# Optimization experiments

Measured on AMD Instinct MI355X. Metric: run time of the kernel, lower is better.

## Reference

```python
import jax, jax.numpy as jnp
import numpy as np

B, C, W, H = 4, 256, 64, 64
CQK = C // 8  # 32


def setup_inputs() -> dict:
    key = jax.random.key(0)
    ks = jax.random.split(key, 8)
    scale = 0.02
    x = jax.random.normal(ks[0], (B, C, W, H), dtype=jnp.float32)
    wq = jax.random.normal(ks[1], (CQK, C), dtype=jnp.float32) * scale
    bq = jnp.zeros((CQK,), dtype=jnp.float32)
    wk = jax.random.normal(ks[2], (CQK, C), dtype=jnp.float32) * scale
    bk = jnp.zeros((CQK,), dtype=jnp.float32)
    wv = jax.random.normal(ks[3], (C, C), dtype=jnp.float32) * scale
    bv = jnp.zeros((C,), dtype=jnp.float32)
    gamma = jnp.zeros((1,), dtype=jnp.float32)
    return {"x": x, "wq": wq, "bq": bq, "wk": wk, "bk": bk,
            "wv": wv, "bv": bv, "gamma": gamma}


def reference(x, wq, bq, wk, bk, wv, bv, gamma):
    b, c, w, h = x.shape
    n = w * h
    xf = x.reshape(b, c, n)                         # b, C, N
    # 1x1 convs == channel matmuls
    q = jnp.einsum('oc,bcn->bno', wq, xf) + bq      # b, N, Cqk
    k = jnp.einsum('oc,bcn->bon', wk, xf) + bk[:, None]  # b, Cqk, N
    v = jnp.einsum('oc,bcn->bon', wv, xf) + bv[:, None]  # b, C, N
    energy = jnp.einsum('bic,bcj->bij', q, k)       # b, N, N
    attention = jax.nn.softmax(energy, axis=-1)     # b, N, N
    # out[b,c,i] = sum_j v[b,c,j] * attention[b,i,j]
    out = jnp.einsum('bcj,bij->bci', v, attention)  # b, C, N
    out = out.reshape(b, c, w, h)
    out = gamma[0] * out + x
    return out, attention
```

## Files before the change

### kernel.cpp

```cpp
#include <hip/hip_runtime.h>

#define NB 4
#define NC 256
#define NN 4096
#define NQK 32

typedef short short8 __attribute__((ext_vector_type(8)));
typedef float f32x4 __attribute__((ext_vector_type(4)));

#define MFMA16(a, b, c) __builtin_amdgcn_mfma_f32_16x16x32_bf16((a), (b), (c), 0, 0, 0)

#if __has_builtin(__builtin_amdgcn_exp2f)
#define EXP2(x) __builtin_amdgcn_exp2f(x)
#else
#define EXP2(x) __expf((x) * 0.6931471805599453f)
#endif

#define L2E 1.4426950408889634f

__device__ __forceinline__ unsigned short f2bf(float f) {
  unsigned int u = __builtin_bit_cast(unsigned int, f);
  u += 0x7fffu + ((u >> 16) & 1u);
  return (unsigned short)(u >> 16);
}
__device__ __forceinline__ float bf2f(unsigned short u) {
  unsigned int v = ((unsigned int)u) << 16;
  return __builtin_bit_cast(float, v);
}

__global__ void k_prep(const float* __restrict__ wq, const float* __restrict__ wk,
                       const float* __restrict__ wv,
                       unsigned short* __restrict__ wqb, unsigned short* __restrict__ wkb,
                       unsigned short* __restrict__ wvb) {
  int i = blockIdx.x * 256 + threadIdx.x;
  if (i < NQK * NC) { wqb[i] = f2bf(wq[i]); wkb[i] = f2bf(wk[i]); }
  wvb[i] = f2bf(wv[i]);
}

__global__ __launch_bounds__(256) void k_proj(
    const float* __restrict__ x,
    const unsigned short* __restrict__ wqb, const unsigned short* __restrict__ wkb,
    const unsigned short* __restrict__ wvb,
    const float* __restrict__ bq, const float* __restrict__ bk,
    const float* __restrict__ bv,
    unsigned short* __restrict__ qb, unsigned short* __restrict__ kTb,
    unsigned short* __restrict__ vb) {
  __shared__ unsigned short ldsx[32][264];
  __shared__ unsigned short ldsvt[256][40];
  int b = blockIdx.y, n0 = blockIdx.x * 32;
  int t = threadIdx.x, w = t >> 6, l = t & 63, lm = l & 15, lk = l >> 4;
  const float* xb = x + (size_t)b * NC * NN + n0;
#pragma unroll
  for (int p = 0; p < 8; ++p) {
    int c = p * 32 + (t >> 3);
    int n4 = (t & 7) * 4;
    f32x4 v4 = *(const f32x4*)(xb + (size_t)c * NN + n4);
#pragma unroll
    for (int u = 0; u < 4; ++u) ldsx[n4 + u][c] = f2bf(v4[u]);
  }
  __syncthreads();
  int s = w & 1, h = w >> 1;
  f32x4 qa[2] = {}, ka[2] = {}, va[10] = {};
  if (h == 0) {
#pragma unroll
    for (int kk = 0; kk < 8; ++kk) {
      short8 a = *(const short8*)(&ldsx[s * 16 + lm][kk * 32 + lk * 8]);
      const unsigned short* wqp = wqb + lm * NC + kk * 32 + lk * 8;
      const unsigned short* wkp = wkb + lm * NC + kk * 32 + lk * 8;
      qa[0] = MFMA16(a, *(const short8*)(wqp), qa[0]);
      qa[1] = MFMA16(a, *(const short8*)(wqp + 16 * NC), qa[1]);
      ka[0] = MFMA16(a, *(const short8*)(wkp), ka[0]);
      ka[1] = MFMA16(a, *(const short8*)(wkp + 16 * NC), ka[1]);
#pragma unroll
      for (int j = 0; j < 6; ++j) {
        const unsigned short* wvp = wvb + (size_t)(j * 16 + lm) * NC + kk * 32 + lk * 8;
        va[j] = MFMA16(a, *(const short8*)(wvp), va[j]);
      }
    }
  } else {
#pragma unroll
    for (int kk = 0; kk < 8; ++kk) {
      short8 a = *(const short8*)(&ldsx[s * 16 + lm][kk * 32 + lk * 8]);
#pragma unroll
      for (int j = 0; j < 10; ++j) {
        const unsigned short* wvp = wvb + (size_t)(96 + j * 16 + lm) * NC + kk * 32 + lk * 8;
        va[j] = MFMA16(a, *(const short8*)(wvp), va[j]);
      }
    }
  }
  if (h == 0) {
    int nrow = n0 + s * 16 + lk * 4;
#pragma unroll
    for (int f = 0; f < 2; ++f) {
      float bqv = bq[f * 16 + lm], bkv = bk[f * 16 + lm];
#pragma unroll
      for (int r = 0; r < 4; ++r) {
        size_t o = ((size_t)(b * NN + nrow + r)) * NQK + f * 16 + lm;
        qb[o] = f2bf((qa[f][r] + bqv) * L2E);
        kTb[o] = f2bf(ka[f][r] + bkv);
      }
    }
#pragma unroll
    for (int j = 0; j < 6; ++j) {
      float bvv = bv[j * 16 + lm];
#pragma unroll
      for (int r = 0; r < 4; ++r)
        ldsvt[j * 16 + lm][s * 16 + lk * 4 + r] = f2bf(va[j][r] + bvv);
    }
  } else {
#pragma unroll
    for (int j = 0; j < 10; ++j) {
      float bvv = bv[96 + j * 16 + lm];
#pragma unroll
      for (int r = 0; r < 4; ++r)
        ldsvt[96 + j * 16 + lm][s * 16 + lk * 4 + r] = f2bf(va[j][r] + bvv);
    }
  }
  __syncthreads();
#pragma unroll
  for (int p = 0; p < 4; ++p) {
    int c = p * 64 + (t >> 2);
    int np = (t & 3) * 8;
    *(short8*)(vb + ((size_t)(b * NC + c)) * NN + n0 + np) =
        *(const short8*)(&ldsvt[c][np]);
  }
}

__global__ __launch_bounds__(512) void k_attn(
    const unsigned short* __restrict__ qb, const unsigned short* __restrict__ kTb,
    const unsigned short* __restrict__ vb, const float* __restrict__ x,
    const float* __restrict__ gamma, float* __restrict__ out,
    float* __restrict__ attn) {
  __shared__ unsigned short ldsv[2][256][72];
  __shared__ unsigned short ldsp[2][64][72];
  __shared__ float ldsd[64][2];
  int id = blockIdx.x;
  int b = (id >> 1) & 3;
  int i0 = (((id >> 3) << 1) | (id & 1)) * 64;
  int t = threadIdx.x, w = t >> 6, l = t & 63, lm = l & 15, lk = l >> 4;
  int is = w & 3, jh = w >> 2;
  int cg = w & 3, ih = w >> 2;
  const f32x4 z = {0.f, 0.f, 0.f, 0.f};

  short8 qa = *(const short8*)(qb + ((size_t)(b * NN + i0 + is * 16 + lm)) * NQK + lk * 8);
  const unsigned short* kbase = kTb + (size_t)b * NN * NQK + lk * 8;

  float ds0[4] = {0.f, 0.f, 0.f, 0.f};
#pragma unroll 4
  for (int j0 = jh * 2048; j0 < jh * 2048 + 2048; j0 += 32) {
    short8 kf0 = *(const short8*)(kbase + (size_t)(j0 + lm) * NQK);
    short8 kf1 = *(const short8*)(kbase + (size_t)(j0 + 16 + lm) * NQK);
    f32x4 e0 = MFMA16(qa, kf0, z);
    f32x4 e1 = MFMA16(qa, kf1, z);
#pragma unroll
    for (int r = 0; r < 4; ++r) ds0[r] += EXP2(e0[r]) + EXP2(e1[r]);
  }
#pragma unroll
  for (int m = 1; m < 16; m <<= 1)
#pragma unroll
    for (int r = 0; r < 4; ++r) ds0[r] += __shfl_xor(ds0[r], m);
  if (lm == 0) {
#pragma unroll
    for (int r = 0; r < 4; ++r) ldsd[is * 16 + lk * 4 + r][jh] = ds0[r];
  }
  __syncthreads();
  float dinv[4];
#pragma unroll
  for (int r = 0; r < 4; ++r) {
    int row = is * 16 + lk * 4 + r;
    dinv[r] = 1.0f / (ldsd[row][0] + ldsd[row][1]);
  }

  f32x4 acc[4][2] = {};
  float g = gamma[0];
  float* attn_b = attn + (size_t)b * NN * NN;
  const unsigned short* vbb = vb + (size_t)b * NC * NN;
  for (int tt = 0; tt < 64; ++tt) {
    int p = tt & 1;
    int j0 = tt * 64;
#pragma unroll
    for (int it = 0; it < 4; ++it) {
      int qid = it * 512 + t;
      int row = qid >> 3, part = qid & 7;
      *(short8*)(&ldsv[p][row][part * 8]) =
          *(const short8*)(vbb + (size_t)row * NN + j0 + part * 8);
    }
    int jb = j0 + jh * 32;
    short8 kf0 = *(const short8*)(kbase + (size_t)(jb + lm) * NQK);
    short8 kf1 = *(const short8*)(kbase + (size_t)(jb + 16 + lm) * NQK);
    f32x4 e0 = MFMA16(qa, kf0, z);
    f32x4 e1 = MFMA16(qa, kf1, z);
#pragma unroll
    for (int r = 0; r < 4; ++r) {
      float p0 = EXP2(e0[r]) * dinv[r];
      float p1 = EXP2(e1[r]) * dinv[r];
      int il = is * 16 + lk * 4 + r;
      ldsp[p][il][jh * 32 + lm] = f2bf(p0);
      ldsp[p][il][jh * 32 + 16 + lm] = f2bf(p1);
    }
    __syncthreads();
#pragma unroll
    for (int q2 = 0; q2 < 2; ++q2) {
      int row = q2 * 32 + (t >> 4);
      int jl = (t & 15) * 4;
      f32x4 vo;
#pragma unroll
      for (int u = 0; u < 4; ++u) vo[u] = bf2f(ldsp[p][row][jl + u]);
      __builtin_nontemporal_store(vo, (f32x4*)(attn_b + (size_t)(i0 + row) * NN + j0 + jl));
    }
#pragma unroll
    for (int kk = 0; kk < 2; ++kk) {
      short8 pf0 = *(const short8*)(&ldsp[p][ih * 32 + lm][kk * 32 + lk * 8]);
      short8 pf1 = *(const short8*)(&ldsp[p][ih * 32 + 16 + lm][kk * 32 + lk * 8]);
#pragma unroll
      for (int ct = 0; ct < 4; ++ct) {
        short8 af = *(const short8*)(&ldsv[p][cg * 64 + ct * 16 + lm][kk * 32 + lk * 8]);
        acc[ct][0] = MFMA16(af, pf0, acc[ct][0]);
        acc[ct][1] = MFMA16(af, pf1, acc[ct][1]);
      }
    }
  }
#pragma unroll
  for (int ct = 0; ct < 4; ++ct)
#pragma unroll
    for (int pt = 0; pt < 2; ++pt)
#pragma unroll
      for (int r = 0; r < 4; ++r) {
        int c = cg * 64 + ct * 16 + lk * 4 + r;
        int i = i0 + ih * 32 + pt * 16 + lm;
        size_t idx = ((size_t)(b * NC + c)) * NN + i;
        out[idx] = g * acc[ct][pt][r] + x[idx];
      }
}

extern "C" void kernel_launch(void* const* d_in, const int* in_sizes, int n_in,
                              void* d_out, int out_size, void* d_ws, size_t ws_size,
                              hipStream_t stream) {
  (void)in_sizes; (void)n_in; (void)out_size; (void)ws_size;
  const float* x  = (const float*)d_in[0];
  const float* wq = (const float*)d_in[1];
  const float* bq = (const float*)d_in[2];
  const float* wk = (const float*)d_in[3];
  const float* bk = (const float*)d_in[4];
  const float* wv = (const float*)d_in[5];
  const float* bv = (const float*)d_in[6];
  const float* gamma = (const float*)d_in[7];
  float* out  = (float*)d_out;
  float* attn = out + (size_t)NB * NC * NN;

  char* ws = (char*)d_ws;
  unsigned short* qb  = (unsigned short*)(ws);
  unsigned short* kTb = (unsigned short*)(ws + 1048576);
  unsigned short* vb  = (unsigned short*)(ws + 2097152);
  unsigned short* wqb = (unsigned short*)(ws + 10485760);
  unsigned short* wkb = (unsigned short*)(ws + 10502144);
  unsigned short* wvb = (unsigned short*)(ws + 10518528);

  k_prep<<<dim3(256), dim3(256), 0, stream>>>(wq, wk, wv, wqb, wkb, wvb);
  k_proj<<<dim3(128, 4), dim3(256), 0, stream>>>(x, wqb, wkb, wvb, bq, bk, bv,
                                                 qb, kTb, vb);
  k_attn<<<dim3(256), dim3(512), 0, stream>>>(qb, kTb, vb, x, gamma, out, attn);
}
```

Measured before the change: 396.0 us.

## Restructure attention kernel with 32x32 MFMA, swizzled LDS, and register-prefetched V

```diff
diff --git a/kernel.cpp b/kernel.cpp
--- a/kernel.cpp
+++ b/kernel.cpp
@@ -5,10 +5,13 @@
 #define NN 4096
 #define NQK 32
 
+typedef short short4v __attribute__((ext_vector_type(4)));
 typedef short short8 __attribute__((ext_vector_type(8)));
 typedef float f32x4 __attribute__((ext_vector_type(4)));
+typedef float f32x16 __attribute__((ext_vector_type(16)));
 
 #define MFMA16(a, b, c) __builtin_amdgcn_mfma_f32_16x16x32_bf16((a), (b), (c), 0, 0, 0)
+#define MFMA32(a, b, c) __builtin_amdgcn_mfma_f32_32x32x16_bf16((a), (b), (c), 0, 0, 0)
 
 #if __has_builtin(__builtin_amdgcn_exp2f)
 #define EXP2(x) __builtin_amdgcn_exp2f(x)
@@ -22,10 +25,6 @@
   unsigned int u = __builtin_bit_cast(unsigned int, f);
   u += 0x7fffu + ((u >> 16) & 1u);
   return (unsigned short)(u >> 16);
-}
-__device__ __forceinline__ float bf2f(unsigned short u) {
-  unsigned int v = ((unsigned int)u) << 16;
-  return __builtin_bit_cast(float, v);
 }
 
 __global__ void k_prep(const float* __restrict__ wq, const float* __restrict__ wk,
@@ -131,106 +130,137 @@
     const unsigned short* __restrict__ vb, const float* __restrict__ x,
     const float* __restrict__ gamma, float* __restrict__ out,
     float* __restrict__ attn) {
-  __shared__ unsigned short ldsv[2][256][72];
-  __shared__ unsigned short ldsp[2][64][72];
-  __shared__ float ldsd[64][2];
+  __shared__ unsigned short ldsv[256 * 64];
+  __shared__ unsigned short ldsp[2][64 * 64];
+  __shared__ float ldsd[64][8];
   int id = blockIdx.x;
   int b = (id >> 1) & 3;
   int i0 = (((id >> 3) << 1) | (id & 1)) * 64;
   int t = threadIdx.x, w = t >> 6, l = t & 63, lm = l & 15, lk = l >> 4;
+  const f32x4 z = {0.f, 0.f, 0.f, 0.f};
+
+  const unsigned short* qbb = qb + ((size_t)(b * NN + i0 + lm)) * NQK + lk * 8;
+  short8 qa0 = *(const short8*)(qbb);
+  short8 qa1 = *(const short8*)(qbb + 16 * NQK);
+  short8 qa2 = *(const short8*)(qbb + 32 * NQK);
+  short8 qa3 = *(const short8*)(qbb + 48 * NQK);
+  const unsigned short* kbase = kTb + (size_t)b * NN * NQK + lk * 8;
+
+  float s0 = 0.f, s1 = 0.f, s2 = 0.f, s3 = 0.f;
+  for (int j0 = w * 512; j0 < w * 512 + 512; j0 += 16) {
+    short8 kf = *(const short8*)(kbase + (size_t)(j0 + lm) * NQK);
+    f32x4 e0 = MFMA16(kf, qa0, z);
+    f32x4 e1 = MFMA16(kf, qa1, z);
+    f32x4 e2 = MFMA16(kf, qa2, z);
+    f32x4 e3 = MFMA16(kf, qa3, z);
+#pragma unroll
+    for (int r = 0; r < 4; ++r) {
+      s0 += EXP2(e0[r]); s1 += EXP2(e1[r]);
+      s2 += EXP2(e2[r]); s3 += EXP2(e3[r]);
+    }
+  }
+  s0 += __shfl_xor(s0, 16); s0 += __shfl_xor(s0, 32);
+  s1 += __shfl_xor(s1, 16); s1 += __shfl_xor(s1, 32);
+  s2 += __shfl_xor(s2, 16); s2 += __shfl_xor(s2, 32);
+  s3 += __shfl_xor(s3, 16); s3 += __shfl_xor(s3, 32);
+  if (lk == 0) {
+    ldsd[lm][w] = s0;       ldsd[16 + lm][w] = s1;
+    ldsd[32 + lm][w] = s2;  ldsd[48 + lm][w] = s3;
+  }
+  __syncthreads();
+
   int is = w & 3, jh = w >> 2;
-  int cg = w & 3, ih = w >> 2;
-  const f32x4 z = {0.f, 0.f, 0.f, 0.f};
-
-  short8 qa = *(const short8*)(qb + ((size_t)(b * NN + i0 + is * 16 + lm)) * NQK + lk * 8);
-  const unsigned short* kbase = kTb + (size_t)b * NN * NQK + lk * 8;
-
-  float ds0[4] = {0.f, 0.f, 0.f, 0.f};
-#pragma unroll 4
-  for (int j0 = jh * 2048; j0 < jh * 2048 + 2048; j0 += 32) {
-    short8 kf0 = *(const short8*)(kbase + (size_t)(j0 + lm) * NQK);
-    short8 kf1 = *(const short8*)(kbase + (size_t)(j0 + 16 + lm) * NQK);
-    f32x4 e0 = MFMA16(qa, kf0, z);
-    f32x4 e1 = MFMA16(qa, kf1, z);
-#pragma unroll
-    for (int r = 0; r < 4; ++r) ds0[r] += EXP2(e0[r]) + EXP2(e1[r]);
-  }
-#pragma unroll
-  for (int m = 1; m < 16; m <<= 1)
-#pragma unroll
-    for (int r = 0; r < 4; ++r) ds0[r] += __shfl_xor(ds0[r], m);
-  if (lm == 0) {
-#pragma unroll
-    for (int r = 0; r < 4; ++r) ldsd[is * 16 + lk * 4 + r][jh] = ds0[r];
-  }
-  __syncthreads();
-  float dinv[4];
-#pragma unroll
-  for (int r = 0; r < 4; ++r) {
-    int row = is * 16 + lk * 4 + r;
-    dinv[r] = 1.0f / (ldsd[row][0] + ldsd[row][1]);
-  }
-
-  f32x4 acc[4][2] = {};
+  int cg = w;
+  short8 qe = (is == 0) ? qa0 : (is == 1) ? qa1 : (is == 2) ? qa2 : qa3;
+  int prow = is * 16 + lm;
+  f32x4 dA = *(const f32x4*)(&ldsd[prow][0]);
+  f32x4 dB = *(const f32x4*)(&ldsd[prow][4]);
+  float dinv = 1.0f / (dA[0] + dA[1] + dA[2] + dA[3] + dB[0] + dB[1] + dB[2] + dB[3]);
+
   float g = gamma[0];
   float* attn_b = attn + (size_t)b * NN * NN;
+  float* aptr = attn_b + (size_t)(i0 + prow) * NN + jh * 32 + lk * 4;
   const unsigned short* vbb = vb + (size_t)b * NC * NN;
+  int vrow = t >> 3, vcol = t & 7;
+  int vx = (vcol * 16) ^ ((vrow & 7) << 4);
+  char* vbase = (char*)ldsv;
+  int pc0 = (jh * 64 + lk * 8) ^ ((prow & 7) << 4);
+  int pc1 = (jh * 64 + lk * 8 + 32) ^ ((prow & 7) << 4);
+  int rowa = cg * 32 + (l & 31);
+  int xa = (rowa & 7) << 4;
+  int xp = ((l & 31) & 7) << 4;
+  int chalf = (l >> 5) * 16;
+  int rp0 = (l & 31) * 128, rp1 = (32 + (l & 31)) * 128;
+
+  short8 vr0 = *(const short8*)(vbb + (size_t)(vrow) * NN + vcol * 8);
+  short8 vr1 = *(const short8*)(vbb + (size_t)(64 + vrow) * NN + vcol * 8);
+  short8 vr2 = *(const short8*)(vbb + (size_t)(128 + vrow) * NN + vcol * 8);
+  short8 vr3 = *(const short8*)(vbb + (size_t)(192 + vrow) * NN + vcol * 8);
+
+  f32x16 acc0 = {}, acc1 = {};
   for (int tt = 0; tt < 64; ++tt) {
     int p = tt & 1;
     int j0 = tt * 64;
-#pragma unroll
-    for (int it = 0; it < 4; ++it) {
-      int qid = it * 512 + t;
-      int row = qid >> 3, part = qid & 7;
-      *(short8*)(&ldsv[p][row][part * 8]) =
-          *(const short8*)(vbb + (size_t)row * NN + j0 + part * 8);
-    }
     int jb = j0 + jh * 32;
     short8 kf0 = *(const short8*)(kbase + (size_t)(jb + lm) * NQK);
     short8 kf1 = *(const short8*)(kbase + (size_t)(jb + 16 + lm) * NQK);
-    f32x4 e0 = MFMA16(qa, kf0, z);
-    f32x4 e1 = MFMA16(qa, kf1, z);
+    f32x4 e0 = MFMA16(kf0, qe, z);
+    f32x4 e1 = MFMA16(kf1, qe, z);
+    f32x4 p0, p1;
 #pragma unroll
     for (int r = 0; r < 4; ++r) {
-      float p0 = EXP2(e0[r]) * dinv[r];
-      float p1 = EXP2(e1[r]) * dinv[r];
-      int il = is * 16 + lk * 4 + r;
-      ldsp[p][il][jh * 32 + lm] = f2bf(p0);
-      ldsp[p][il][jh * 32 + 16 + lm] = f2bf(p1);
-    }
+      p0[r] = EXP2(e0[r]) * dinv;
+      p1[r] = EXP2(e1[r]) * dinv;
+    }
+    __builtin_nontemporal_store(p0, (f32x4*)(aptr + j0));
+    __builtin_nontemporal_store(p1, (f32x4*)(aptr + j0 + 16));
+    short4v pb0, pb1;
+#pragma unroll
+    for (int r = 0; r < 4; ++r) {
+      pb0[r] = (short)f2bf(p0[r]);
+      pb1[r] = (short)f2bf(p1[r]);
+    }
+    char* pb = (char*)(&ldsp[p][0]) + prow * 128;
+    *(short4v*)(pb + pc0) = pb0;
+    *(short4v*)(pb + pc1) = pb1;
     __syncthreads();
-#pragma unroll
-    for (int q2 = 0; q2 < 2; ++q2) {
-      int row = q2 * 32 + (t >> 4);
-      int jl = (t & 15) * 4;
-      f32x4 vo;
-#pragma unroll
-      for (int u = 0; u < 4; ++u) vo[u] = bf2f(ldsp[p][row][jl + u]);
-      __builtin_nontemporal_store(vo, (f32x4*)(attn_b + (size_t)(i0 + row) * NN + j0 + jl));
-    }
-#pragma unroll
-    for (int kk = 0; kk < 2; ++kk) {
-      short8 pf0 = *(const short8*)(&ldsp[p][ih * 32 + lm][kk * 32 + lk * 8]);
-      short8 pf1 = *(const short8*)(&ldsp[p][ih * 32 + 16 + lm][kk * 32 + lk * 8]);
-#pragma unroll
-      for (int ct = 0; ct < 4; ++ct) {
-        short8 af = *(const short8*)(&ldsv[p][cg * 64 + ct * 16 + lm][kk * 32 + lk * 8]);
-        acc[ct][0] = MFMA16(af, pf0, acc[ct][0]);
-        acc[ct][1] = MFMA16(af, pf1, acc[ct][1]);
-      }
-    }
-  }
-#pragma unroll
-  for (int ct = 0; ct < 4; ++ct)
-#pragma unroll
-    for (int pt = 0; pt < 2; ++pt)
-#pragma unroll
-      for (int r = 0; r < 4; ++r) {
-        int c = cg * 64 + ct * 16 + lk * 4 + r;
-        int i = i0 + ih * 32 + pt * 16 + lm;
-        size_t idx = ((size_t)(b * NC + c)) * NN + i;
-        out[idx] = g * acc[ct][pt][r] + x[idx];
-      }
+    *(short8*)(vbase + (vrow) * 128 + vx) = vr0;
+    *(short8*)(vbase + (64 + vrow) * 128 + vx) = vr1;
+    *(short8*)(vbase + (128 + vrow) * 128 + vx) = vr2;
+    *(short8*)(vbase + (192 + vrow) * 128 + vx) = vr3;
+    {
+      size_t jn = (size_t)(((tt + 1) & 63) * 64);
+      vr0 = *(const short8*)(vbb + (size_t)(vrow) * NN + jn + vcol * 8);
+      vr1 = *(const short8*)(vbb + (size_t)(64 + vrow) * NN + jn + vcol * 8);
+      vr2 = *(const short8*)(vbb + (size_t)(128 + vrow) * NN + jn + vcol * 8);
+      vr3 = *(const short8*)(vbb + (size_t)(192 + vrow) * NN + jn + vcol * 8);
+    }
+    __syncthreads();
+    const char* pvp = (const char*)(&ldsp[p][0]);
+    const char* abase = vbase + rowa * 128;
+    __builtin_amdgcn_s_setprio(1);
+#pragma unroll
+    for (int kk = 0; kk < 4; ++kk) {
+      int cb = kk * 32 + chalf;
+      short8 af = *(const short8*)(abase + (cb ^ xa));
+      short8 pf0 = *(const short8*)(pvp + rp0 + (cb ^ xp));
+      short8 pf1 = *(const short8*)(pvp + rp1 + (cb ^ xp));
+      acc0 = MFMA32(af, pf0, acc0);
+      acc1 = MFMA32(af, pf1, acc1);
+    }
+    __builtin_amdgcn_s_setprio(0);
+  }
+
+  int ieg0 = i0 + (l & 31), ieg1 = i0 + 32 + (l & 31);
+  int crb = cg * 32 + 4 * (l >> 5);
+#pragma unroll
+  for (int reg = 0; reg < 16; ++reg) {
+    int c = crb + (reg & 3) + 8 * (reg >> 2);
+    size_t o0 = ((size_t)(b * NC + c)) * NN + ieg0;
+    size_t o1 = ((size_t)(b * NC + c)) * NN + ieg1;
+    out[o0] = g * acc0[reg] + x[o0];
+    out[o1] = g * acc1[reg] + x[o1];
+  }
 }
 
 extern "C" void kernel_launch(void* const* d_in, const int* in_sizes, int n_in,
```

Result: faster. 374.0 us (-5.6%).
